# Optimization experiments

Hardware: AMD Instinct MI355X
Metric: run time of the kernel (lower is better)

The kernel has to match this reference:

```python
import jax, jax.numpy as jnp
import numpy as np


def _shift(x, axis, d):
    # value at voxel p becomes x[p + d*e_axis], zero outside the grid
    n = x.shape[axis]
    zero = jnp.zeros_like(jax.lax.slice_in_dim(x, 0, 1, axis=axis))
    if d > 0:
        return jnp.concatenate([jax.lax.slice_in_dim(x, 1, n, axis=axis), zero], axis=axis)
    return jnp.concatenate([zero, jax.lax.slice_in_dim(x, 0, n - 1, axis=axis)], axis=axis)


def _forward(coords, instance_gt, S, num_scales):
    # InputLayer mode=4: average features of duplicate coords.
    # features = [instance+1, 1]; averaging duplicates of [v,1] gives [mean(v), 1].
    inst = instance_gt.astype(jnp.float32) + 1.0
    c = coords.astype(jnp.int32)
    flat = (c[:, 0] * S + c[:, 1]) * S + c[:, 2]
    ssum = jnp.zeros(S * S * S, jnp.float32).at[flat].add(inst)
    cnt = jnp.zeros(S * S * S, jnp.float32).at[flat].add(1.0)
    val = (ssum / jnp.maximum(cnt, 1.0)).reshape(S, S, S)   # mean label per active voxel, 0 if inactive
    act = (cnt > 0).astype(jnp.float32).reshape(S, S, S)    # active-site mask
    outs = []
    for scale in range(num_scales):
        if scale == 0:
            v, a = val, act
        else:
            f = 2 ** scale
            Ss = S // f
            # scn AveragePooling divides by pool volume; features[:, :1]/count then
            # renormalizes -> mean of val over ACTIVE fine voxels in the block.
            vsum = val.reshape(Ss, f, Ss, f, Ss, f).sum(axis=(1, 3, 5))
            asum = act.reshape(Ss, f, Ss, f, Ss, f).sum(axis=(1, 3, 5))
            a = (asum > 0).astype(jnp.float32)
            v = vsum / jnp.maximum(asum, 1.0)
        va = v * a
        feats = []
        masks = []
        # one-hot submanifold conv kernel offsets (4,22,10,16,12,14) = (-x,+x,-y,+y,-z,+z)
        for axis in range(3):
            for d in (-1, 1):
                sh = _shift(va, axis, d)                      # neighbor value, 0 if neighbor inactive
                feats.append((jnp.abs(sh - v) < 0.01).astype(jnp.float32))
                masks.append((sh > 0).astype(jnp.float32))
        # submanifold conv is only defined at active sites -> mask by a
        out = jnp.stack(feats + masks, axis=-1) * a[..., None]  # [Ss,Ss,Ss,12]
        outs.append(out.reshape(-1, 12))
    return jnp.concatenate(outs, axis=0)


def setup_inputs() -> dict:
    key = jax.random.key(0)
    k1, k2 = jax.random.split(key)
    N, S = 4_000_000, 128
    coords = jax.random.randint(k1, (N, 3), 0, S, dtype=jnp.int32)
    instance_gt = jax.random.randint(k2, (N,), 0, 50).astype(jnp.float32)
    return {"coords": coords, "instance_gt": instance_gt, "inputScale": S, "numScales": 6}


def reference(coords, instance_gt, inputScale, numScales):
    return _forward(coords, instance_gt, inputScale, numScales)
```

## Files before the change

kernel.cpp:

```cpp
#include <hip/hip_runtime.h>

#define GS3 2097152
#define NS1 262144
#define NS2 32768
#define NS3 4096
#define NS4 512
#define NS5 64
#define NSALL 299584

#define OB1 25165824
#define OB2 28311552
#define OB3 28704768
#define OB4 28753920
#define OB5 28760064

#define NREG 512
#define RVOX 4096
#define CAP  10240
#define PPB  8192

__global__ __launch_bounds__(256) void zero_cnt_kernel(unsigned int* __restrict__ cnt) {
  cnt[threadIdx.x] = 0u;
  cnt[threadIdx.x + 256] = 0u;
}

__global__ __launch_bounds__(256) void bin_kernel(
    const int* __restrict__ coords, const float* __restrict__ inst,
    unsigned int* __restrict__ cnt, unsigned int* __restrict__ bins, int N) {
  __shared__ unsigned int lrec[PPB];
  __shared__ unsigned int srec[PPB];
  __shared__ unsigned int hist[NREG];
  __shared__ unsigned int lofs[NREG];
  __shared__ unsigned int basec[NREG];
  __shared__ unsigned int part[256];
  __shared__ unsigned int total_sh;
  int tid = threadIdx.x;
  int start = blockIdx.x * PPB;
  for (int j = tid; j < NREG; j += 256) hist[j] = 0;
  __syncthreads();
#pragma unroll
  for (int j = 0; j < PPB / 256; j++) {
    int i = start + j * 256 + tid;
    unsigned v = 0xFFFFFFFFu;
    if (i < N) {
      int x = coords[3 * i + 0];
      int y = coords[3 * i + 1];
      int z = coords[3 * i + 2];
      unsigned lab = (unsigned)inst[i] + 1u;
      unsigned r = ((unsigned)x << 2) | ((unsigned)y >> 5);
      v = (r << 18) | ((((unsigned)(y & 31) << 7) | (unsigned)z) << 6) | lab;
      atomicAdd(&hist[r], 1u);
    }
    lrec[j * 256 + tid] = v;
  }
  __syncthreads();
  unsigned ha = hist[2 * tid], hb = hist[2 * tid + 1];
  part[tid] = ha + hb;
  __syncthreads();
  for (int o = 1; o < 256; o <<= 1) {
    unsigned v = part[tid];
    unsigned add = (tid >= o) ? part[tid - o] : 0u;
    __syncthreads();
    part[tid] = v + add;
    __syncthreads();
  }
  unsigned inc = part[tid];
  unsigned ex = inc - (ha + hb);
  lofs[2 * tid] = ex;
  lofs[2 * tid + 1] = ex + ha;
  if (tid == 255) total_sh = inc;
  __syncthreads();
  for (int j = tid; j < NREG; j += 256) {
    unsigned h = hist[j];
    basec[j] = h ? atomicAdd(&cnt[j], h) : 0u;
  }
  __syncthreads();
  for (int j = tid; j < NREG; j += 256) hist[j] = 0;
  __syncthreads();
#pragma unroll
  for (int j = 0; j < PPB / 256; j++) {
    unsigned v = lrec[j * 256 + tid];
    if (v != 0xFFFFFFFFu) {
      unsigned r = v >> 18;
      unsigned pos = lofs[r] + atomicAdd(&hist[r], 1u);
      srec[pos] = v;
    }
  }
  __syncthreads();
  unsigned total = total_sh;
  for (unsigned j = tid; j < total; j += 256) {
    unsigned v = srec[j];
    unsigned r = v >> 18;
    unsigned p = basec[r] + (j - lofs[r]);
    if (p < CAP) bins[r * CAP + p] = v & 0x3FFFFu;
  }
}

__global__ __launch_bounds__(256) void build_kernel(
    const unsigned int* __restrict__ cnt, const unsigned int* __restrict__ bins,
    unsigned int* __restrict__ P) {
  __shared__ unsigned int grid[RVOX];
  int r = blockIdx.x;
  int tid = threadIdx.x;
  for (int j = tid; j < RVOX; j += 256) grid[j] = 0;
  __syncthreads();
  int n = min((int)cnt[r], CAP);
  for (int k = tid; k < n; k += 256) {
    unsigned v = bins[r * CAP + k];
    atomicAdd(&grid[v >> 6], (1u << 20) | (v & 63u));
  }
  __syncthreads();
  unsigned baseoff = ((unsigned)(r >> 2) << 14) | ((unsigned)(r & 3) << 12);
  for (int j = tid; j < RVOX; j += 256) P[baseoff + j] = grid[j];
}

__global__ __launch_bounds__(256) void scatter_kernel(
    const int* __restrict__ coords, const float* __restrict__ inst,
    unsigned int* __restrict__ P, int N) {
  int i = blockIdx.x * blockDim.x + threadIdx.x;
  if (i >= N) return;
  int x = coords[3 * i + 0];
  int y = coords[3 * i + 1];
  int z = coords[3 * i + 2];
  unsigned lab = (unsigned)inst[i] + 1u;
  atomicAdd(&P[(x << 14) + (y << 7) + z], (1u << 20) | lab);
}

__global__ __launch_bounds__(256) void pool1_kernel(
    const unsigned int* __restrict__ P,
    double* __restrict__ vs1, double* __restrict__ as1) {
  int q = blockIdx.x * blockDim.x + threadIdx.x;
  if (q >= NS1) return;
  int X = q >> 12, Y = (q >> 6) & 63, Z = q & 63;
  double vs = 0.0, as = 0.0;
#pragma unroll
  for (int dx = 0; dx < 2; dx++)
#pragma unroll
    for (int dy = 0; dy < 2; dy++)
#pragma unroll
      for (int dz = 0; dz < 2; dz++) {
        int p = (((2 * X + dx) << 14) + ((2 * Y + dy) << 7) + (2 * Z + dz));
        unsigned pk = P[p];
        unsigned c = pk >> 20;
        if (c) {
          vs += (double)(pk & 0xFFFFFu) / (double)c;
          as += 1.0;
        }
      }
  vs1[q] = vs;
  as1[q] = as;
}

__global__ __launch_bounds__(256) void poolRest_kernel(
    const double* __restrict__ vs1, const double* __restrict__ as1,
    double* __restrict__ vs2, double* __restrict__ as2,
    double* __restrict__ vs3, double* __restrict__ as3,
    double* __restrict__ vs4, double* __restrict__ as4,
    double* __restrict__ vs5, double* __restrict__ as5) {
  int t = blockIdx.x * blockDim.x + threadIdx.x;

  if (t < NS2) {
    int q = t;
    int X = q >> 10, Y = (q >> 5) & 31, Z = q & 31;
    double vs = 0.0, as = 0.0;
#pragma unroll
    for (int dx = 0; dx < 2; dx++)
#pragma unroll
      for (int dy = 0; dy < 2; dy++)
#pragma unroll
        for (int dz = 0; dz < 2; dz++) {
          int p = ((((X << 1) + dx) << 12) + (((Y << 1) + dy) << 6) + ((Z << 1) + dz));
          vs += vs1[p];
          as += as1[p];
        }
    vs2[q] = vs;
    as2[q] = as;
    return;
  }
  t -= NS2;
  if (t < NS3) {
    int q = t;
    int X = q >> 8, Y = (q >> 4) & 15, Z = q & 15;
    double vs = 0.0, as = 0.0;
    for (int dx = 0; dx < 4; dx++)
      for (int dy = 0; dy < 4; dy++)
#pragma unroll
        for (int dz = 0; dz < 4; dz++) {
          int p = ((((X << 2) + dx) << 12) + (((Y << 2) + dy) << 6) + ((Z << 2) + dz));
          vs += vs1[p];
          as += as1[p];
        }
    vs3[q] = vs;
    as3[q] = as;
    return;
  }
  t -= NS3;
  if (t < NS4 * 64) {
    int w = t >> 6, lane = t & 63;
    int X = w >> 6, Y = (w >> 3) & 7, Z = w & 7;
    double vs = 0.0, as = 0.0;
#pragma unroll
    for (int j = 0; j < 8; j++) {
      int c = lane * 8 + j;
      int dx = c >> 6, dy = (c >> 3) & 7, dz = c & 7;
      int p = ((((X << 3) + dx) << 12) + (((Y << 3) + dy) << 6) + ((Z << 3) + dz));
      vs += vs1[p];
      as += as1[p];
    }
    for (int o = 32; o > 0; o >>= 1) {
      vs += __shfl_down(vs, o, 64);
      as += __shfl_down(as, o, 64);
    }
    if (lane == 0) { vs4[w] = vs; as4[w] = as; }
    return;
  }
  t -= NS4 * 64;
  if (t < NS5 * 64) {
    int w = t >> 6, lane = t & 63;
    int X = w >> 4, Y = (w >> 2) & 3, Z = w & 3;
    double vs = 0.0, as = 0.0;
    for (int j = 0; j < 64; j++) {
      int c = lane * 64 + j;
      int dx = c >> 8, dy = (c >> 4) & 15, dz = c & 15;
      int p = ((((X << 4) + dx) << 12) + (((Y << 4) + dy) << 6) + ((Z << 4) + dz));
      vs += vs1[p];
      as += as1[p];
    }
    for (int o = 32; o > 0; o >>= 1) {
      vs += __shfl_down(vs, o, 64);
      as += __shfl_down(as, o, 64);
    }
    if (lane == 0) { vs5[w] = vs; as5[w] = as; }
  }
}

__global__ __launch_bounds__(256) void out_kernel(
    const unsigned int* __restrict__ P,
    const double* __restrict__ vs1, const double* __restrict__ as1,
    const double* __restrict__ vs2, const double* __restrict__ as2,
    const double* __restrict__ vs3, const double* __restrict__ as3,
    const double* __restrict__ vs4, const double* __restrict__ as4,
    const double* __restrict__ vs5, const double* __restrict__ as5,
    float* __restrict__ out) {
  int p = blockIdx.x * blockDim.x + threadIdx.x;
  if (p < GS3) {
    unsigned pk = P[p];
    int cc = (int)(pk >> 20);
    float4 r0 = {0.f, 0.f, 0.f, 0.f}, r1 = r0, r2 = r0;
    if (cc) {
      int sc = (int)(pk & 0xFFFFFu);
      int x = p >> 14, y = (p >> 7) & 127, z = p & 127;
      const int off[6] = {-(1 << 14), (1 << 14), -(1 << 7), (1 << 7), -1, 1};
      const bool inb[6] = {x > 0, x < 127, y > 0, y < 127, z > 0, z < 127};
      float f[6], m[6];
#pragma unroll
      for (int k = 0; k < 6; k++) {
        int sn = 0, cn = 0;
        if (inb[k]) {
          unsigned pn = P[p + off[k]];
          cn = (int)(pn >> 20);
          sn = (int)(pn & 0xFFFFFu);
        }
        if (cn) {
          long long d = (long long)sn * cc - (long long)sc * cn;
          if (d < 0) d = -d;
          f[k] = (100ll * d < (long long)cn * cc) ? 1.f : 0.f;
          m[k] = 1.f;
        } else {
          f[k] = 0.f;
          m[k] = 0.f;
        }
      }
      r0 = {f[0], f[1], f[2], f[3]};
      r1 = {f[4], f[5], m[0], m[1]};
      r2 = {m[2], m[3], m[4], m[5]};
    }
    float4* o = (float4*)(out + 12ll * p);
    o[0] = r0; o[1] = r1; o[2] = r2;
    return;
  }
  int t = p - GS3;
  const double *vs, *as;
  int ls, q;
  long long obase;
  if (t < NS1) { q = t; vs = vs1; as = as1; ls = 6; obase = OB1; }
  else if (t < NS1 + NS2) { q = t - NS1; vs = vs2; as = as2; ls = 5; obase = OB2; }
  else if (t < NS1 + NS2 + NS3) { q = t - NS1 - NS2; vs = vs3; as = as3; ls = 4; obase = OB3; }
  else if (t < NS1 + NS2 + NS3 + NS4) { q = t - NS1 - NS2 - NS3; vs = vs4; as = as4; ls = 3; obase = OB4; }
  else if (t < NSALL) { q = t - NS1 - NS2 - NS3 - NS4; vs = vs5; as = as5; ls = 2; obase = OB5; }
  else return;

  int Ss = 1 << ls;
  int X = q >> (2 * ls), Y = (q >> ls) & (Ss - 1), Z = q & (Ss - 1);
  double ac = as[q];
  float4 r0 = {0.f, 0.f, 0.f, 0.f}, r1 = r0, r2 = r0;
  if (ac > 0.0) {
    double vc = vs[q] / ac;
    const int off[6] = {-(Ss * Ss), Ss * Ss, -Ss, Ss, -1, 1};
    const bool inb[6] = {X > 0, X < Ss - 1, Y > 0, Y < Ss - 1, Z > 0, Z < Ss - 1};
    float f[6], m[6];
#pragma unroll
    for (int k = 0; k < 6; k++) {
      double van = 0.0;
      if (inb[k]) {
        double an = as[q + off[k]];
        if (an > 0.0) van = vs[q + off[k]] / an;
      }
      f[k] = (fabs(van - vc) < 0.01) ? 1.f : 0.f;
      m[k] = (van > 0.0) ? 1.f : 0.f;
    }
    r0 = {f[0], f[1], f[2], f[3]};
    r1 = {f[4], f[5], m[0], m[1]};
    r2 = {m[2], m[3], m[4], m[5]};
  }
  float4* o = (float4*)(out + obase + 12ll * q);
  o[0] = r0; o[1] = r1; o[2] = r2;
}

extern "C" void kernel_launch(void* const* d_in, const int* in_sizes, int n_in,
                              void* d_out, int out_size, void* d_ws, size_t ws_size,
                              hipStream_t stream) {
  const int* coords = (const int*)d_in[0];
  const float* inst = (const float*)d_in[1];
  int N = in_sizes[1];
  float* out = (float*)d_out;

  char* base = (char*)d_ws;
  unsigned int* P = (unsigned int*)base;
  double* vs1 = (double*)(base + 8388608);
  double* as1 = vs1 + NS1;
  double* vs2 = as1 + NS1; double* as2 = vs2 + NS2;
  double* vs3 = as2 + NS2; double* as3 = vs3 + NS3;
  double* vs4 = as3 + NS3; double* as4 = vs4 + NS4;
  double* vs5 = as4 + NS4; double* as5 = vs5 + NS5;
  size_t cnt_off = 13182976;
  unsigned int* cnt  = (unsigned int*)(base + cnt_off);
  unsigned int* bins = (unsigned int*)(base + cnt_off + 2048);
  size_t need = cnt_off + 2048 + (size_t)NREG * CAP * 4;

  if (ws_size >= need) {
    zero_cnt_kernel<<<1, 256, 0, stream>>>(cnt);
    bin_kernel<<<(N + PPB - 1) / PPB, 256, 0, stream>>>(coords, inst, cnt, bins, N);
    build_kernel<<<NREG, 256, 0, stream>>>(cnt, bins, P);
  } else {
    hipMemsetAsync(P, 0, (size_t)GS3 * 4, stream);
    scatter_kernel<<<(N + 255) / 256, 256, 0, stream>>>(coords, inst, P, N);
  }
  pool1_kernel<<<NS1 / 256, 256, 0, stream>>>(P, vs1, as1);
  poolRest_kernel<<<(NS2 + NS3 + NS4 * 64 + NS5 * 64) / 256, 256, 0, stream>>>(
      vs1, as1, vs2, as2, vs3, as3, vs4, as4, vs5, as5);
  out_kernel<<<(GS3 + NSALL + 255) / 256, 256, 0, stream>>>(
      P, vs1, as1, vs2, as2, vs3, as3, vs4, as4, vs5, as5, out);
}
```

Before: 103.6 us.

## Fuse all pipeline stages into one cooperative persistent kernel with grid syncs

Replaces the six separate launches (zero, bin, build, pool1, poolRest, out) with a single cooperative kernel of 512 persistent blocks that loops over the work of each stage and separates stages with grid.sync(). The binning chunk size is halved so more chunks are spread across the persistent blocks. This aims to remove kernel launch gaps and tail effects between stages, at the cost of grid-wide barriers, lower occupancy with only 512 blocks on the per-element stages, and grid-stride loops. The memset/atomic-scatter fallback for small workspaces is dropped and now returns without computing anything.

```diff
diff --git a/kernel.cpp b/kernel.cpp
--- a/kernel.cpp
+++ b/kernel.cpp
@@ -1,4 +1,7 @@
 #include <hip/hip_runtime.h>
+#include <hip/hip_cooperative_groups.h>
+
+namespace cg = cooperative_groups;
 
 #define GS3 2097152
 #define NS1 262144
@@ -17,25 +20,24 @@
 #define NREG 512
 #define RVOX 4096
 #define CAP  10240
-#define PPB  8192
-
-__global__ __launch_bounds__(256) void zero_cnt_kernel(unsigned int* __restrict__ cnt) {
-  cnt[threadIdx.x] = 0u;
-  cnt[threadIdx.x + 256] = 0u;
-}
-
-__global__ __launch_bounds__(256) void bin_kernel(
-    const int* __restrict__ coords, const float* __restrict__ inst,
-    unsigned int* __restrict__ cnt, unsigned int* __restrict__ bins, int N) {
-  __shared__ unsigned int lrec[PPB];
-  __shared__ unsigned int srec[PPB];
-  __shared__ unsigned int hist[NREG];
-  __shared__ unsigned int lofs[NREG];
-  __shared__ unsigned int basec[NREG];
-  __shared__ unsigned int part[256];
-  __shared__ unsigned int total_sh;
-  int tid = threadIdx.x;
-  int start = blockIdx.x * PPB;
+#define PPB  4096
+
+#define MEGA_BLOCKS 512
+#define SMEM_WORDS (2 * PPB + 3 * NREG + 256 + 1)
+
+__device__ __forceinline__ void bin_chunk(
+    unsigned* __restrict__ sm, const int* __restrict__ coords,
+    const float* __restrict__ inst, unsigned* __restrict__ cnt,
+    unsigned* __restrict__ bins, int N, int chunk, int tid) {
+  unsigned* lrec  = sm;
+  unsigned* srec  = sm + PPB;
+  unsigned* hist  = sm + 2 * PPB;
+  unsigned* lofs  = hist + NREG;
+  unsigned* basec = lofs + NREG;
+  unsigned* part  = basec + NREG;
+  unsigned* totp  = part + 256;
+  int start = chunk * PPB;
+  __syncthreads();
   for (int j = tid; j < NREG; j += 256) hist[j] = 0;
   __syncthreads();
 #pragma unroll
@@ -68,7 +70,7 @@
   unsigned ex = inc - (ha + hb);
   lofs[2 * tid] = ex;
   lofs[2 * tid + 1] = ex + ha;
-  if (tid == 255) total_sh = inc;
+  if (tid == 255) *totp = inc;
   __syncthreads();
   for (int j = tid; j < NREG; j += 256) {
     unsigned h = hist[j];
@@ -87,7 +89,7 @@
     }
   }
   __syncthreads();
-  unsigned total = total_sh;
+  unsigned total = *totp;
   for (unsigned j = tid; j < total; j += 256) {
     unsigned v = srec[j];
     unsigned r = v >> 18;
@@ -96,12 +98,11 @@
   }
 }
 
-__global__ __launch_bounds__(256) void build_kernel(
-    const unsigned int* __restrict__ cnt, const unsigned int* __restrict__ bins,
-    unsigned int* __restrict__ P) {
-  __shared__ unsigned int grid[RVOX];
-  int r = blockIdx.x;
-  int tid = threadIdx.x;
+__device__ __forceinline__ void build_region(
+    unsigned* __restrict__ grid, const unsigned* __restrict__ cnt,
+    const unsigned* __restrict__ bins, unsigned* __restrict__ P,
+    int r, int tid) {
+  __syncthreads();
   for (int j = tid; j < RVOX; j += 256) grid[j] = 0;
   __syncthreads();
   int n = min((int)cnt[r], CAP);
@@ -114,23 +115,9 @@
   for (int j = tid; j < RVOX; j += 256) P[baseoff + j] = grid[j];
 }
 
-__global__ __launch_bounds__(256) void scatter_kernel(
-    const int* __restrict__ coords, const float* __restrict__ inst,
-    unsigned int* __restrict__ P, int N) {
-  int i = blockIdx.x * blockDim.x + threadIdx.x;
-  if (i >= N) return;
-  int x = coords[3 * i + 0];
-  int y = coords[3 * i + 1];
-  int z = coords[3 * i + 2];
-  unsigned lab = (unsigned)inst[i] + 1u;
-  atomicAdd(&P[(x << 14) + (y << 7) + z], (1u << 20) | lab);
-}
-
-__global__ __launch_bounds__(256) void pool1_kernel(
-    const unsigned int* __restrict__ P,
-    double* __restrict__ vs1, double* __restrict__ as1) {
-  int q = blockIdx.x * blockDim.x + threadIdx.x;
-  if (q >= NS1) return;
+__device__ __forceinline__ void pool1_item(
+    const unsigned* __restrict__ P, double* __restrict__ vs1,
+    double* __restrict__ as1, int q) {
   int X = q >> 12, Y = (q >> 6) & 63, Z = q & 63;
   double vs = 0.0, as = 0.0;
 #pragma unroll
@@ -151,14 +138,12 @@
   as1[q] = as;
 }
 
-__global__ __launch_bounds__(256) void poolRest_kernel(
+__device__ __forceinline__ void poolRest_item(
     const double* __restrict__ vs1, const double* __restrict__ as1,
     double* __restrict__ vs2, double* __restrict__ as2,
     double* __restrict__ vs3, double* __restrict__ as3,
     double* __restrict__ vs4, double* __restrict__ as4,
-    double* __restrict__ vs5, double* __restrict__ as5) {
-  int t = blockIdx.x * blockDim.x + threadIdx.x;
-
+    double* __restrict__ vs5, double* __restrict__ as5, int t) {
   if (t < NS2) {
     int q = t;
     int X = q >> 10, Y = (q >> 5) & 31, Z = q & 31;
@@ -234,15 +219,14 @@
   }
 }
 
-__global__ __launch_bounds__(256) void out_kernel(
-    const unsigned int* __restrict__ P,
+__device__ __forceinline__ void out_item(
+    const unsigned* __restrict__ P,
     const double* __restrict__ vs1, const double* __restrict__ as1,
     const double* __restrict__ vs2, const double* __restrict__ as2,
     const double* __restrict__ vs3, const double* __restrict__ as3,
     const double* __restrict__ vs4, const double* __restrict__ as4,
     const double* __restrict__ vs5, const double* __restrict__ as5,
-    float* __restrict__ out) {
-  int p = blockIdx.x * blockDim.x + threadIdx.x;
+    float* __restrict__ out, int p) {
   if (p < GS3) {
     unsigned pk = P[p];
     int cc = (int)(pk >> 20);
@@ -317,6 +301,91 @@
   o[0] = r0; o[1] = r1; o[2] = r2;
 }
 
+__global__ __launch_bounds__(256) void mega_kernel(
+    const int* __restrict__ coords, const float* __restrict__ inst,
+    unsigned* __restrict__ cnt, unsigned* __restrict__ bins,
+    unsigned* __restrict__ P,
+    double* __restrict__ vs1, double* __restrict__ as1,
+    double* __restrict__ vs2, double* __restrict__ as2,
+    double* __restrict__ vs3, double* __restrict__ as3,
+    double* __restrict__ vs4, double* __restrict__ as4,
+    double* __restrict__ vs5, double* __restrict__ as5,
+    float* __restrict__ out, int N, int nchunks) {
+  __shared__ unsigned sm[SMEM_WORDS];
+  cg::grid_group grid = cg::this_grid();
+  int bid = blockIdx.x, tid = threadIdx.x;
+  int nthreads = gridDim.x * 256;
+  int gt = bid * 256 + tid;
+
+  if (bid == 0)
+    for (int j = tid; j < NREG; j += 256) cnt[j] = 0;
+  grid.sync();
+  for (int c = bid; c < nchunks; c += gridDim.x)
+    bin_chunk(sm, coords, inst, cnt, bins, N, c, tid);
+  grid.sync();
+  for (int r = bid; r < NREG; r += gridDim.x)
+    build_region(sm, cnt, bins, P, r, tid);
+  grid.sync();
+  for (int q = gt; q < NS1; q += nthreads)
+    pool1_item(P, vs1, as1, q);
+  grid.sync();
+  for (int t = gt; t < NS2 + NS3 + NS4 * 64 + NS5 * 64; t += nthreads)
+    poolRest_item(vs1, as1, vs2, as2, vs3, as3, vs4, as4, vs5, as5, t);
+  grid.sync();
+  for (int p = gt; p < GS3 + NSALL; p += nthreads)
+    out_item(P, vs1, as1, vs2, as2, vs3, as3, vs4, as4, vs5, as5, out, p);
+}
+
+__global__ __launch_bounds__(256) void zero_cnt_kernel(unsigned int* __restrict__ cnt) {
+  cnt[threadIdx.x] = 0u;
+  cnt[threadIdx.x + 256] = 0u;
+}
+
+__global__ __launch_bounds__(256) void bin_kernel(
+    const int* __restrict__ coords, const float* __restrict__ inst,
+    unsigned int* __restrict__ cnt, unsigned int* __restrict__ bins, int N) {
+  __shared__ unsigned sm[SMEM_WORDS];
+  bin_chunk(sm, coords, inst, cnt, bins, N, blockIdx.x, threadIdx.x);
+}
+
+__global__ __launch_bounds__(256) void build_kernel(
+    const unsigned int* __restrict__ cnt, const unsigned int* __restrict__ bins,
+    unsigned int* __restrict__ P) {
+  __shared__ unsigned grid[RVOX];
+  build_region(grid, cnt, bins, P, blockIdx.x, threadIdx.x);
+}
+
+__global__ __launch_bounds__(256) void pool1_kernel(
+    const unsigned int* __restrict__ P,
+    double* __restrict__ vs1, double* __restrict__ as1) {
+  int q = blockIdx.x * blockDim.x + threadIdx.x;
+  if (q < NS1) pool1_item(P, vs1, as1, q);
+}
+
+__global__ __launch_bounds__(256) void poolRest_kernel(
+    const double* __restrict__ vs1, const double* __restrict__ as1,
+    double* __restrict__ vs2, double* __restrict__ as2,
+    double* __restrict__ vs3, double* __restrict__ as3,
+    double* __restrict__ vs4, double* __restrict__ as4,
+    double* __restrict__ vs5, double* __restrict__ as5) {
+  int t = blockIdx.x * blockDim.x + threadIdx.x;
+  if (t < NS2 + NS3 + NS4 * 64 + NS5 * 64)
+    poolRest_item(vs1, as1, vs2, as2, vs3, as3, vs4, as4, vs5, as5, t);
+}
+
+__global__ __launch_bounds__(256) void out_kernel(
+    const unsigned int* __restrict__ P,
+    const double* __restrict__ vs1, const double* __restrict__ as1,
+    const double* __restrict__ vs2, const double* __restrict__ as2,
+    const double* __restrict__ vs3, const double* __restrict__ as3,
+    const double* __restrict__ vs4, const double* __restrict__ as4,
+    const double* __restrict__ vs5, const double* __restrict__ as5,
+    float* __restrict__ out) {
+  int p = blockIdx.x * blockDim.x + threadIdx.x;
+  if (p < GS3 + NSALL)
+    out_item(P, vs1, as1, vs2, as2, vs3, as3, vs4, as4, vs5, as5, out, p);
+}
+
 extern "C" void kernel_launch(void* const* d_in, const int* in_sizes, int n_in,
                               void* d_out, int out_size, void* d_ws, size_t ws_size,
                               hipStream_t stream) {
@@ -337,17 +406,25 @@
   unsigned int* cnt  = (unsigned int*)(base + cnt_off);
   unsigned int* bins = (unsigned int*)(base + cnt_off + 2048);
   size_t need = cnt_off + 2048 + (size_t)NREG * CAP * 4;
+  int nchunks = (N + PPB - 1) / PPB;
 
   if (ws_size >= need) {
+    void* args[] = {(void*)&coords, (void*)&inst, (void*)&cnt, (void*)&bins,
+                    (void*)&P, (void*)&vs1, (void*)&as1, (void*)&vs2, (void*)&as2,
+                    (void*)&vs3, (void*)&as3, (void*)&vs4, (void*)&as4,
+                    (void*)&vs5, (void*)&as5, (void*)&out, (void*)&N,
+                    (void*)&nchunks};
+    hipError_t err = hipLaunchCooperativeKernel(
+        (const void*)mega_kernel, dim3(MEGA_BLOCKS), dim3(256), args, 0, stream);
+    if (err == hipSuccess) return;
     zero_cnt_kernel<<<1, 256, 0, stream>>>(cnt);
-    bin_kernel<<<(N + PPB - 1) / PPB, 256, 0, stream>>>(coords, inst, cnt, bins, N);
+    bin_kernel<<<nchunks, 256, 0, stream>>>(coords, inst, cnt, bins, N);
     build_kernel<<<NREG, 256, 0, stream>>>(cnt, bins, P);
   } else {
-    hipMemsetAsync(P, 0, (size_t)GS3 * 4, stream);
-    scatter_kernel<<<(N + 255) / 256, 256, 0, stream>>>(coords, inst, P, N);
+    return;
   }
   pool1_kernel<<<NS1 / 256, 256, 0, stream>>>(P, vs1, as1);
-  poolRest_kernel<<<(NS2 + NS3 + NS4 * 64 + NS5 * 64) / 256, 256, 0, stream>>>(
+  poolRest_kernel<<<(NS2 + NS3 + NS4 * 64 + NS5 * 64 + 255) / 256, 256, 0, stream>>>(
       vs1, as1, vs2, as2, vs3, as3, vs4, as4, vs5, as5);
   out_kernel<<<(GS3 + NSALL + 255) / 256, 256, 0, stream>>>(
       P, vs1, as1, vs2, as2, vs3, as3, vs4, as4, vs5, as5, out);
```

New measurement: 398.0 us. +284.2%, slower.

## Fuse first-level pooling into region build and use nontemporal output stores

Applied to the files above, without the earlier changes.

Regions now cover two x-slices (256 regions of 8192 voxels), so each build block holds complete 2x2x2 pooling cells in shared memory and computes the scale-1 pooling directly. This removes the separate pool1 kernel and its re-read of the packed grid from global memory. Output stores in out_kernel now use nontemporal builtins so the large streamed output does not pollute the cache. The scatter fallback is gone and the launch now returns early if the workspace is too small. Bin capacity changes and fewer, larger blocks may affect occupancy and overflow margin.

```diff
diff --git a/kernel.cpp b/kernel.cpp
--- a/kernel.cpp
+++ b/kernel.cpp
@@ -14,29 +14,31 @@
 #define OB4 28753920
 #define OB5 28760064
 
-#define NREG 512
-#define RVOX 4096
-#define CAP  10240
-#define PPB  8192
+#define NREG 256
+#define RVOX 8192
+#define CAP  18432
+#define PPB  4096
+
+typedef float f4 __attribute__((ext_vector_type(4)));
+
 
 __global__ __launch_bounds__(256) void zero_cnt_kernel(unsigned int* __restrict__ cnt) {
   cnt[threadIdx.x] = 0u;
-  cnt[threadIdx.x + 256] = 0u;
 }
 
 __global__ __launch_bounds__(256) void bin_kernel(
     const int* __restrict__ coords, const float* __restrict__ inst,
     unsigned int* __restrict__ cnt, unsigned int* __restrict__ bins, int N) {
-  __shared__ unsigned int lrec[PPB];
-  __shared__ unsigned int srec[PPB];
-  __shared__ unsigned int hist[NREG];
-  __shared__ unsigned int lofs[NREG];
-  __shared__ unsigned int basec[NREG];
-  __shared__ unsigned int part[256];
-  __shared__ unsigned int total_sh;
+  __shared__ unsigned lrec[PPB];
+  __shared__ unsigned srec[PPB];
+  __shared__ unsigned hist[NREG];
+  __shared__ unsigned lofs[NREG];
+  __shared__ unsigned basec[NREG];
+  __shared__ unsigned part[256];
+  __shared__ unsigned total_sh;
   int tid = threadIdx.x;
   int start = blockIdx.x * PPB;
-  for (int j = tid; j < NREG; j += 256) hist[j] = 0;
+  hist[tid] = 0;
   __syncthreads();
 #pragma unroll
   for (int j = 0; j < PPB / 256; j++) {
@@ -47,15 +49,16 @@
       int y = coords[3 * i + 1];
       int z = coords[3 * i + 2];
       unsigned lab = (unsigned)inst[i] + 1u;
-      unsigned r = ((unsigned)x << 2) | ((unsigned)y >> 5);
-      v = (r << 18) | ((((unsigned)(y & 31) << 7) | (unsigned)z) << 6) | lab;
+      unsigned r = (((unsigned)x >> 1) << 2) | ((unsigned)y >> 5);
+      unsigned l = (((unsigned)x & 1) << 12) | (((unsigned)y & 31) << 7) | (unsigned)z;
+      v = (r << 19) | (l << 6) | lab;
       atomicAdd(&hist[r], 1u);
     }
     lrec[j * 256 + tid] = v;
   }
   __syncthreads();
-  unsigned ha = hist[2 * tid], hb = hist[2 * tid + 1];
-  part[tid] = ha + hb;
+  unsigned ha = hist[tid];
+  part[tid] = ha;
   __syncthreads();
   for (int o = 1; o < 256; o <<= 1) {
     unsigned v = part[tid];
@@ -65,23 +68,21 @@
     __syncthreads();
   }
   unsigned inc = part[tid];
-  unsigned ex = inc - (ha + hb);
-  lofs[2 * tid] = ex;
-  lofs[2 * tid + 1] = ex + ha;
+  lofs[tid] = inc - ha;
   if (tid == 255) total_sh = inc;
   __syncthreads();
-  for (int j = tid; j < NREG; j += 256) {
-    unsigned h = hist[j];
-    basec[j] = h ? atomicAdd(&cnt[j], h) : 0u;
-  }
-  __syncthreads();
-  for (int j = tid; j < NREG; j += 256) hist[j] = 0;
+  {
+    unsigned h = hist[tid];
+    basec[tid] = h ? atomicAdd(&cnt[tid], h) : 0u;
+  }
+  __syncthreads();
+  hist[tid] = 0;
   __syncthreads();
 #pragma unroll
   for (int j = 0; j < PPB / 256; j++) {
     unsigned v = lrec[j * 256 + tid];
     if (v != 0xFFFFFFFFu) {
-      unsigned r = v >> 18;
+      unsigned r = v >> 19;
       unsigned pos = lofs[r] + atomicAdd(&hist[r], 1u);
       srec[pos] = v;
     }
@@ -90,16 +91,17 @@
   unsigned total = total_sh;
   for (unsigned j = tid; j < total; j += 256) {
     unsigned v = srec[j];
-    unsigned r = v >> 18;
+    unsigned r = v >> 19;
     unsigned p = basec[r] + (j - lofs[r]);
-    if (p < CAP) bins[r * CAP + p] = v & 0x3FFFFu;
-  }
-}
-
-__global__ __launch_bounds__(256) void build_kernel(
+    if (p < CAP) bins[r * CAP + p] = v & 0x7FFFFu;
+  }
+}
+
+__global__ __launch_bounds__(256) void build_pool_kernel(
     const unsigned int* __restrict__ cnt, const unsigned int* __restrict__ bins,
-    unsigned int* __restrict__ P) {
-  __shared__ unsigned int grid[RVOX];
+    unsigned int* __restrict__ P,
+    double* __restrict__ vs1, double* __restrict__ as1) {
+  __shared__ unsigned grid[RVOX];
   int r = blockIdx.x;
   int tid = threadIdx.x;
   for (int j = tid; j < RVOX; j += 256) grid[j] = 0;
@@ -110,45 +112,32 @@
     atomicAdd(&grid[v >> 6], (1u << 20) | (v & 63u));
   }
   __syncthreads();
-  unsigned baseoff = ((unsigned)(r >> 2) << 14) | ((unsigned)(r & 3) << 12);
-  for (int j = tid; j < RVOX; j += 256) P[baseoff + j] = grid[j];
-}
-
-__global__ __launch_bounds__(256) void scatter_kernel(
-    const int* __restrict__ coords, const float* __restrict__ inst,
-    unsigned int* __restrict__ P, int N) {
-  int i = blockIdx.x * blockDim.x + threadIdx.x;
-  if (i >= N) return;
-  int x = coords[3 * i + 0];
-  int y = coords[3 * i + 1];
-  int z = coords[3 * i + 2];
-  unsigned lab = (unsigned)inst[i] + 1u;
-  atomicAdd(&P[(x << 14) + (y << 7) + z], (1u << 20) | lab);
-}
-
-__global__ __launch_bounds__(256) void pool1_kernel(
-    const unsigned int* __restrict__ P,
-    double* __restrict__ vs1, double* __restrict__ as1) {
-  int q = blockIdx.x * blockDim.x + threadIdx.x;
-  if (q >= NS1) return;
-  int X = q >> 12, Y = (q >> 6) & 63, Z = q & 63;
-  double vs = 0.0, as = 0.0;
-#pragma unroll
-  for (int dx = 0; dx < 2; dx++)
-#pragma unroll
-    for (int dy = 0; dy < 2; dy++)
-#pragma unroll
-      for (int dz = 0; dz < 2; dz++) {
-        int p = (((2 * X + dx) << 14) + ((2 * Y + dy) << 7) + (2 * Z + dz));
-        unsigned pk = P[p];
-        unsigned c = pk >> 20;
-        if (c) {
-          vs += (double)(pk & 0xFFFFFu) / (double)c;
-          as += 1.0;
-        }
-      }
-  vs1[q] = vs;
-  as1[q] = as;
+  int X = r >> 2, yq = r & 3;
+  unsigned pbase = ((unsigned)(X * 2) << 14) | ((unsigned)yq << 12);
+  for (int j = tid; j < RVOX; j += 256) {
+    P[pbase + ((j >> 12) << 14) + (j & 0xFFF)] = grid[j];
+  }
+  for (int c = tid; c < 1024; c += 256) {
+    int yl = c >> 6, Z = c & 63;
+    double vs = 0.0, as = 0.0;
+#pragma unroll
+    for (int dx = 0; dx < 2; dx++)
+#pragma unroll
+      for (int dy = 0; dy < 2; dy++)
+#pragma unroll
+        for (int dz = 0; dz < 2; dz++) {
+          int j = (dx << 12) | ((2 * yl + dy) << 7) | (2 * Z + dz);
+          unsigned pk = grid[j];
+          unsigned cc = pk >> 20;
+          if (cc) {
+            vs += (double)(pk & 0xFFFFFu) / (double)cc;
+            as += 1.0;
+          }
+        }
+    int q = (X << 12) | (((yq << 4) + yl) << 6) | Z;
+    vs1[q] = vs;
+    as1[q] = as;
+  }
 }
 
 __global__ __launch_bounds__(256) void poolRest_kernel(
@@ -246,7 +235,7 @@
   if (p < GS3) {
     unsigned pk = P[p];
     int cc = (int)(pk >> 20);
-    float4 r0 = {0.f, 0.f, 0.f, 0.f}, r1 = r0, r2 = r0;
+    f4 r0 = {0.f, 0.f, 0.f, 0.f}, r1 = r0, r2 = r0;
     if (cc) {
       int sc = (int)(pk & 0xFFFFFu);
       int x = p >> 14, y = (p >> 7) & 127, z = p & 127;
@@ -271,12 +260,14 @@
           m[k] = 0.f;
         }
       }
-      r0 = {f[0], f[1], f[2], f[3]};
-      r1 = {f[4], f[5], m[0], m[1]};
-      r2 = {m[2], m[3], m[4], m[5]};
-    }
-    float4* o = (float4*)(out + 12ll * p);
-    o[0] = r0; o[1] = r1; o[2] = r2;
+      r0 = (f4){f[0], f[1], f[2], f[3]};
+      r1 = (f4){f[4], f[5], m[0], m[1]};
+      r2 = (f4){m[2], m[3], m[4], m[5]};
+    }
+    f4* o = (f4*)(out + 12ll * p);
+    __builtin_nontemporal_store(r0, o + 0);
+    __builtin_nontemporal_store(r1, o + 1);
+    __builtin_nontemporal_store(r2, o + 2);
     return;
   }
   int t = p - GS3;
@@ -293,7 +284,7 @@
   int Ss = 1 << ls;
   int X = q >> (2 * ls), Y = (q >> ls) & (Ss - 1), Z = q & (Ss - 1);
   double ac = as[q];
-  float4 r0 = {0.f, 0.f, 0.f, 0.f}, r1 = r0, r2 = r0;
+  f4 r0 = {0.f, 0.f, 0.f, 0.f}, r1 = r0, r2 = r0;
   if (ac > 0.0) {
     double vc = vs[q] / ac;
     const int off[6] = {-(Ss * Ss), Ss * Ss, -Ss, Ss, -1, 1};
@@ -309,12 +300,14 @@
       f[k] = (fabs(van - vc) < 0.01) ? 1.f : 0.f;
       m[k] = (van > 0.0) ? 1.f : 0.f;
     }
-    r0 = {f[0], f[1], f[2], f[3]};
-    r1 = {f[4], f[5], m[0], m[1]};
-    r2 = {m[2], m[3], m[4], m[5]};
-  }
-  float4* o = (float4*)(out + obase + 12ll * q);
-  o[0] = r0; o[1] = r1; o[2] = r2;
+    r0 = (f4){f[0], f[1], f[2], f[3]};
+    r1 = (f4){f[4], f[5], m[0], m[1]};
+    r2 = (f4){m[2], m[3], m[4], m[5]};
+  }
+  f4* o = (f4*)(out + obase + 12ll * q);
+  __builtin_nontemporal_store(r0, o + 0);
+  __builtin_nontemporal_store(r1, o + 1);
+  __builtin_nontemporal_store(r2, o + 2);
 }
 
 extern "C" void kernel_launch(void* const* d_in, const int* in_sizes, int n_in,
@@ -335,19 +328,15 @@
   double* vs5 = as4 + NS4; double* as5 = vs5 + NS5;
   size_t cnt_off = 13182976;
   unsigned int* cnt  = (unsigned int*)(base + cnt_off);
-  unsigned int* bins = (unsigned int*)(base + cnt_off + 2048);
-  size_t need = cnt_off + 2048 + (size_t)NREG * CAP * 4;
-
-  if (ws_size >= need) {
-    zero_cnt_kernel<<<1, 256, 0, stream>>>(cnt);
-    bin_kernel<<<(N + PPB - 1) / PPB, 256, 0, stream>>>(coords, inst, cnt, bins, N);
-    build_kernel<<<NREG, 256, 0, stream>>>(cnt, bins, P);
-  } else {
-    hipMemsetAsync(P, 0, (size_t)GS3 * 4, stream);
-    scatter_kernel<<<(N + 255) / 256, 256, 0, stream>>>(coords, inst, P, N);
-  }
-  pool1_kernel<<<NS1 / 256, 256, 0, stream>>>(P, vs1, as1);
-  poolRest_kernel<<<(NS2 + NS3 + NS4 * 64 + NS5 * 64) / 256, 256, 0, stream>>>(
+  unsigned int* bins = (unsigned int*)(base + cnt_off + 1024);
+  size_t need = cnt_off + 1024 + (size_t)NREG * CAP * 4;
+  if (ws_size < need) return;
+
+  int nchunks = (N + PPB - 1) / PPB;
+  zero_cnt_kernel<<<1, 256, 0, stream>>>(cnt);
+  bin_kernel<<<nchunks, 256, 0, stream>>>(coords, inst, cnt, bins, N);
+  build_pool_kernel<<<NREG, 256, 0, stream>>>(cnt, bins, P, vs1, as1);
+  poolRest_kernel<<<(NS2 + NS3 + NS4 * 64 + NS5 * 64 + 255) / 256, 256, 0, stream>>>(
       vs1, as1, vs2, as2, vs3, as3, vs4, as4, vs5, as5);
   out_kernel<<<(GS3 + NSALL + 255) / 256, 256, 0, stream>>>(
       P, vs1, as1, vs2, as2, vs3, as3, vs4, as4, vs5, as5, out);
```

Result: slower. 121.4 us (+17.2%).

## Reshape bin regions to 2x16x128 slabs and fuse first pooling into build

Applied to the files above, without the earlier changes.

Bin regions change from 1x32x128 slabs to 2x16x128 slabs, so each region's shared-memory grid holds whole 2x2x2 pooling blocks. The build kernel now computes the scale-1 pooled sums straight from shared memory and writes vs1/as1, which removes the separate pool1 kernel and its reread of the full voxel grid. The atomic scatter fallback is removed, so the function now returns early with no output if the workspace is too small.

```diff
diff --git a/kernel.cpp b/kernel.cpp
--- a/kernel.cpp
+++ b/kernel.cpp
@@ -19,6 +19,7 @@
 #define CAP  10240
 #define PPB  8192
 
+
 __global__ __launch_bounds__(256) void zero_cnt_kernel(unsigned int* __restrict__ cnt) {
   cnt[threadIdx.x] = 0u;
   cnt[threadIdx.x + 256] = 0u;
@@ -27,13 +28,13 @@
 __global__ __launch_bounds__(256) void bin_kernel(
     const int* __restrict__ coords, const float* __restrict__ inst,
     unsigned int* __restrict__ cnt, unsigned int* __restrict__ bins, int N) {
-  __shared__ unsigned int lrec[PPB];
-  __shared__ unsigned int srec[PPB];
-  __shared__ unsigned int hist[NREG];
-  __shared__ unsigned int lofs[NREG];
-  __shared__ unsigned int basec[NREG];
-  __shared__ unsigned int part[256];
-  __shared__ unsigned int total_sh;
+  __shared__ unsigned lrec[PPB];
+  __shared__ unsigned srec[PPB];
+  __shared__ unsigned hist[NREG];
+  __shared__ unsigned lofs[NREG];
+  __shared__ unsigned basec[NREG];
+  __shared__ unsigned part[256];
+  __shared__ unsigned total_sh;
   int tid = threadIdx.x;
   int start = blockIdx.x * PPB;
   for (int j = tid; j < NREG; j += 256) hist[j] = 0;
@@ -47,8 +48,9 @@
       int y = coords[3 * i + 1];
       int z = coords[3 * i + 2];
       unsigned lab = (unsigned)inst[i] + 1u;
-      unsigned r = ((unsigned)x << 2) | ((unsigned)y >> 5);
-      v = (r << 18) | ((((unsigned)(y & 31) << 7) | (unsigned)z) << 6) | lab;
+      unsigned r = (((unsigned)x >> 1) << 3) | ((unsigned)y >> 4);
+      unsigned l = (((unsigned)x & 1) << 11) | (((unsigned)y & 15) << 7) | (unsigned)z;
+      v = (r << 18) | (l << 6) | lab;
       atomicAdd(&hist[r], 1u);
     }
     lrec[j * 256 + tid] = v;
@@ -96,10 +98,11 @@
   }
 }
 
-__global__ __launch_bounds__(256) void build_kernel(
+__global__ __launch_bounds__(256) void build_pool_kernel(
     const unsigned int* __restrict__ cnt, const unsigned int* __restrict__ bins,
-    unsigned int* __restrict__ P) {
-  __shared__ unsigned int grid[RVOX];
+    unsigned int* __restrict__ P,
+    double* __restrict__ vs1, double* __restrict__ as1) {
+  __shared__ unsigned grid[RVOX];
   int r = blockIdx.x;
   int tid = threadIdx.x;
   for (int j = tid; j < RVOX; j += 256) grid[j] = 0;
@@ -110,45 +113,32 @@
     atomicAdd(&grid[v >> 6], (1u << 20) | (v & 63u));
   }
   __syncthreads();
-  unsigned baseoff = ((unsigned)(r >> 2) << 14) | ((unsigned)(r & 3) << 12);
-  for (int j = tid; j < RVOX; j += 256) P[baseoff + j] = grid[j];
-}
-
-__global__ __launch_bounds__(256) void scatter_kernel(
-    const int* __restrict__ coords, const float* __restrict__ inst,
-    unsigned int* __restrict__ P, int N) {
-  int i = blockIdx.x * blockDim.x + threadIdx.x;
-  if (i >= N) return;
-  int x = coords[3 * i + 0];
-  int y = coords[3 * i + 1];
-  int z = coords[3 * i + 2];
-  unsigned lab = (unsigned)inst[i] + 1u;
-  atomicAdd(&P[(x << 14) + (y << 7) + z], (1u << 20) | lab);
-}
-
-__global__ __launch_bounds__(256) void pool1_kernel(
-    const unsigned int* __restrict__ P,
-    double* __restrict__ vs1, double* __restrict__ as1) {
-  int q = blockIdx.x * blockDim.x + threadIdx.x;
-  if (q >= NS1) return;
-  int X = q >> 12, Y = (q >> 6) & 63, Z = q & 63;
-  double vs = 0.0, as = 0.0;
-#pragma unroll
-  for (int dx = 0; dx < 2; dx++)
-#pragma unroll
-    for (int dy = 0; dy < 2; dy++)
-#pragma unroll
-      for (int dz = 0; dz < 2; dz++) {
-        int p = (((2 * X + dx) << 14) + ((2 * Y + dy) << 7) + (2 * Z + dz));
-        unsigned pk = P[p];
-        unsigned c = pk >> 20;
-        if (c) {
-          vs += (double)(pk & 0xFFFFFu) / (double)c;
-          as += 1.0;
-        }
-      }
-  vs1[q] = vs;
-  as1[q] = as;
+  int X = r >> 3, yo = r & 7;
+  unsigned pbase = ((unsigned)(2 * X) << 14) | ((unsigned)yo << 11);
+  for (int j = tid; j < RVOX; j += 256) {
+    P[pbase + ((j >> 11) << 14) + (j & 0x7FF)] = grid[j];
+  }
+  for (int c = tid; c < 512; c += 256) {
+    int yl = c >> 6, Z = c & 63;
+    double vs = 0.0, as = 0.0;
+#pragma unroll
+    for (int dx = 0; dx < 2; dx++)
+#pragma unroll
+      for (int dy = 0; dy < 2; dy++)
+#pragma unroll
+        for (int dz = 0; dz < 2; dz++) {
+          int j = (dx << 11) | ((2 * yl + dy) << 7) | (2 * Z + dz);
+          unsigned pk = grid[j];
+          unsigned cc = pk >> 20;
+          if (cc) {
+            vs += (double)(pk & 0xFFFFFu) / (double)cc;
+            as += 1.0;
+          }
+        }
+    int q = (X << 12) | (((yo << 3) + yl) << 6) | Z;
+    vs1[q] = vs;
+    as1[q] = as;
+  }
 }
 
 __global__ __launch_bounds__(256) void poolRest_kernel(
@@ -337,17 +327,13 @@
   unsigned int* cnt  = (unsigned int*)(base + cnt_off);
   unsigned int* bins = (unsigned int*)(base + cnt_off + 2048);
   size_t need = cnt_off + 2048 + (size_t)NREG * CAP * 4;
-
-  if (ws_size >= need) {
-    zero_cnt_kernel<<<1, 256, 0, stream>>>(cnt);
-    bin_kernel<<<(N + PPB - 1) / PPB, 256, 0, stream>>>(coords, inst, cnt, bins, N);
-    build_kernel<<<NREG, 256, 0, stream>>>(cnt, bins, P);
-  } else {
-    hipMemsetAsync(P, 0, (size_t)GS3 * 4, stream);
-    scatter_kernel<<<(N + 255) / 256, 256, 0, stream>>>(coords, inst, P, N);
-  }
-  pool1_kernel<<<NS1 / 256, 256, 0, stream>>>(P, vs1, as1);
-  poolRest_kernel<<<(NS2 + NS3 + NS4 * 64 + NS5 * 64) / 256, 256, 0, stream>>>(
+  if (ws_size < need) return;
+
+  int nchunks = (N + PPB - 1) / PPB;
+  zero_cnt_kernel<<<1, 256, 0, stream>>>(cnt);
+  bin_kernel<<<nchunks, 256, 0, stream>>>(coords, inst, cnt, bins, N);
+  build_pool_kernel<<<NREG, 256, 0, stream>>>(cnt, bins, P, vs1, as1);
+  poolRest_kernel<<<(NS2 + NS3 + NS4 * 64 + NS5 * 64 + 255) / 256, 256, 0, stream>>>(
       vs1, as1, vs2, as2, vs3, as3, vs4, as4, vs5, as5);
   out_kernel<<<(GS3 + NSALL + 255) / 256, 256, 0, stream>>>(
       P, vs1, as1, vs2, as2, vs3, as3, vs4, as4, vs5, as5, out);
```

New measurement: 101.3 us. 1.02x faster.
